# Kernel optimization log

Hardware: AMD Instinct MI355X
Metric: run time of the kernel (lower is better)

Reference implementation:

```python
import jax, jax.numpy as jnp
import numpy as np

EPS = 1e-12  # torch F.normalize eps


def setup_inputs() -> dict:
    key = jax.random.key(0)
    k1, k2, k3 = jax.random.split(key, 3)
    B, D, H, W, K = 64, 512, 32, 32, 64
    x = jax.random.normal(k1, (B, D, H, W), dtype=jnp.float32)
    w = jax.random.normal(k2, (K, D), dtype=jnp.float32) * 0.05  # 1x1 conv weight
    c = jax.random.normal(k3, (K, D), dtype=jnp.float32)          # cluster centers
    return {"x": x, "w": w, "c": c}


def reference(x, w, c):
    B, D, H, W = x.shape
    K = w.shape[0]
    N = H * W
    # 1x1 conv (no bias): (B,D,H,W) x (K,D) -> (B,K,H,W)
    features = jnp.einsum('bdhw,kd->bkhw', x, w)
    # NOTE: original applies softmax over dim=2 (the H axis only)
    a_bar = jax.nn.softmax(features, axis=2)
    xf = x.reshape(B, D, N)
    a = a_bar.reshape(B, K, N)
    # V[b,k,d] = sum_n a[b,k,n] * (x[b,d,n] - c[k,d])
    V = jnp.einsum('bkn,bdn->bkd', a, xf) - a.sum(axis=2)[:, :, None] * c[None]
    V = V.transpose(2, 1, 0)  # (D, K, B)
    # F.normalize(V, p=2, dim=1) applied twice (second is idempotent)
    norm = jnp.maximum(jnp.linalg.norm(V, axis=1, keepdims=True), EPS)
    y = V / norm
    norm2 = jnp.maximum(jnp.linalg.norm(y, axis=1, keepdims=True), EPS)
    return y / norm2
```

## Files before the change

kernel.cpp:

```cpp
#include <hip/hip_runtime.h>


typedef __attribute__((ext_vector_type(8))) short short8;
typedef __attribute__((ext_vector_type(4))) float f32x4;
typedef unsigned short u16;
typedef unsigned int u32;

union S8u { u32 q[4]; short8 s; };

__device__ __forceinline__ u32 pk2(float lo, float hi) {
  union { float f; u32 u; } a, b; a.f = lo; b.f = hi;
  u32 xl = (a.u + 0x7fffu + ((a.u >> 16) & 1u)) >> 16;
  u32 xh = (b.u + 0x7fffu + ((b.u >> 16) & 1u)) & 0xffff0000u;
  return xl | xh;
}

__device__ __forceinline__ u16 bf1(float f) {
  union { float f; u32 u; } a; a.f = f;
  return (u16)((a.u + 0x7fffu + ((a.u >> 16) & 1u)) >> 16);
}

__global__ __launch_bounds__(256, 2) void k1_features(
    const float* __restrict__ x, const float* __restrict__ wgt,
    float* __restrict__ feat)
{
  const int blk = blockIdx.x;
  const int b = blk & 63, ntile = blk >> 6;
  const int tid = threadIdx.x, lane = tid & 63, wv = tid >> 6;
  const int row = lane & 15, q = lane >> 4;
  const int nb = ntile * 128 + wv * 32;
  const float* xb = x + ((size_t)b << 19);

  f32x4 acc[4][2];
#pragma unroll
  for (int mt = 0; mt < 4; mt++)
#pragma unroll
    for (int nt = 0; nt < 2; nt++) acc[mt][nt] = (f32x4){0.f, 0.f, 0.f, 0.f};

#pragma unroll 2
  for (int d0 = 0; d0 < 512; d0 += 32) {
    short8 af[4];
#pragma unroll
    for (int mt = 0; mt < 4; mt++) {
      const float* pw = wgt + (mt * 16 + row) * 512 + d0 + q * 8;
      f32x4 w0 = *(const f32x4*)pw;
      f32x4 w1 = *(const f32x4*)(pw + 4);
      S8u t;
      t.q[0] = pk2(w0[0], w0[1]); t.q[1] = pk2(w0[2], w0[3]);
      t.q[2] = pk2(w1[0], w1[1]); t.q[3] = pk2(w1[2], w1[3]);
      af[mt] = t.s;
    }
    short8 bf[2];
#pragma unroll
    for (int nt = 0; nt < 2; nt++) {
      const float* px = xb + (size_t)(d0 + q * 8) * 1024 + nb + nt * 16 + row;
      float v0 = px[0],    v1 = px[1024], v2 = px[2048], v3 = px[3072];
      float v4 = px[4096], v5 = px[5120], v6 = px[6144], v7 = px[7168];
      S8u t;
      t.q[0] = pk2(v0, v1); t.q[1] = pk2(v2, v3);
      t.q[2] = pk2(v4, v5); t.q[3] = pk2(v6, v7);
      bf[nt] = t.s;
    }
#pragma unroll
    for (int nt = 0; nt < 2; nt++)
#pragma unroll
      for (int mt = 0; mt < 4; mt++)
        acc[mt][nt] = __builtin_amdgcn_mfma_f32_16x16x32_bf16(af[mt], bf[nt], acc[mt][nt], 0, 0, 0);
  }
  float* fb = feat + ((size_t)b << 16);
#pragma unroll
  for (int mt = 0; mt < 4; mt++)
#pragma unroll
    for (int nt = 0; nt < 2; nt++)
#pragma unroll
      for (int r = 0; r < 4; r++)
        fb[(mt * 16 + q * 4 + r) * 1024 + nb + nt * 16 + row] = acc[mt][nt][r];
}

__global__ __launch_bounds__(256) void k1b_softmax(
    const float* __restrict__ feat, u16* __restrict__ am)
{
  const int tid = threadIdx.x, lane = tid & 63, wv = tid >> 6;
  const int rid = blockIdx.x * 4 + wv;
  const float* f = feat + ((size_t)rid << 10);
  u16* ar = am + ((size_t)rid << 10);
  const int w = lane & 31, half = lane >> 5;
  const int base = w + half * 512;
  float v[16];
  float m = -1e30f;
#pragma unroll
  for (int i = 0; i < 16; i++) { v[i] = f[base + i * 32]; m = fmaxf(m, v[i]); }
  m = fmaxf(m, __shfl_xor(m, 32));
  float s = 0.f;
#pragma unroll
  for (int i = 0; i < 16; i++) { v[i] = __expf(v[i] - m); s += v[i]; }
  s += __shfl_xor(s, 32);
  const float inv = 1.0f / s;
#pragma unroll
  for (int i = 0; i < 16; i++) ar[base + i * 32] = bf1(v[i] * inv);
}

__global__ __launch_bounds__(256, 2) void k2_aggregate(
    const float* __restrict__ x, const u16* __restrict__ am,
    const float* __restrict__ cc, float* __restrict__ yw)
{
  const int blk = blockIdx.x;
  const int b = blk & 63, dt = blk >> 6;
  const int tid = threadIdx.x, lane = tid & 63, wv = tid >> 6;
  const int row = lane & 15, q = lane >> 4;
  const int drow = dt * 64 + wv * 16 + row;
  const float* xb = x + ((size_t)b << 19);
  const u16* ab = am + ((size_t)b << 16);

  f32x4 acc[4];
#pragma unroll
  for (int mt = 0; mt < 4; mt++) acc[mt] = (f32x4){0.f, 0.f, 0.f, 0.f};

#pragma unroll 2
  for (int n0 = 0; n0 < 1024; n0 += 32) {
    short8 bfr;
    {
      const float* px = xb + (size_t)drow * 1024 + n0 + q * 8;
      f32x4 g0 = *(const f32x4*)px;
      f32x4 g1 = *(const f32x4*)(px + 4);
      S8u t;
      t.q[0] = pk2(g0[0], g0[1]); t.q[1] = pk2(g0[2], g0[3]);
      t.q[2] = pk2(g1[0], g1[1]); t.q[3] = pk2(g1[2], g1[3]);
      bfr = t.s;
    }
#pragma unroll
    for (int mt = 0; mt < 4; mt++) {
      short8 af = *(const short8*)(ab + (mt * 16 + row) * 1024 + n0 + q * 8);
      acc[mt] = __builtin_amdgcn_mfma_f32_16x16x32_bf16(af, bfr, acc[mt], 0, 0, 0);
    }
  }
  const int dcol = dt * 64 + wv * 16 + row;
  float v[16]; float ss = 0.f;
#pragma unroll
  for (int mt = 0; mt < 4; mt++)
#pragma unroll
    for (int r = 0; r < 4; r++) {
      const int k = mt * 16 + q * 4 + r;
      const float t = acc[mt][r] - 32.0f * cc[k * 512 + dcol];
      v[mt * 4 + r] = t; ss += t * t;
    }
  ss += __shfl_xor(ss, 16);
  ss += __shfl_xor(ss, 32);
  const float rn = 1.0f / fmaxf(sqrtf(ss), 1e-12f);
  float* yb = yw + ((size_t)b << 15) + dcol;
#pragma unroll
  for (int mt = 0; mt < 4; mt++)
#pragma unroll
    for (int r = 0; r < 4; r++)
      yb[(size_t)(mt * 16 + q * 4 + r) << 9] = v[mt * 4 + r] * rn;
}

__global__ __launch_bounds__(256) void k3_transpose(
    const float* __restrict__ yw, float* __restrict__ out)
{
  const int blk = blockIdx.x;
  const int k = blk & 63;
  const int dt = blk >> 6;
  const int d0 = dt * 64;
  const int tid = threadIdx.x;
  __shared__ float T[64][68];
  {
    const int bl = tid >> 2, seg = tid & 3;
    const float* src = yw + (size_t)bl * 32768 + k * 512 + d0 + seg * 16;
#pragma unroll
    for (int i = 0; i < 4; i++) {
      f32x4 v = *(const f32x4*)(src + i * 4);
#pragma unroll
      for (int jj = 0; jj < 4; jj++) T[seg * 16 + i * 4 + jj][bl] = v[jj];
    }
  }
  __syncthreads();
  {
    const int dl = tid >> 2, bseg = tid & 3;
    float* dst = out + (size_t)(d0 + dl) * 4096 + k * 64 + bseg * 16;
    const float* srcT = &T[dl][bseg * 16];
#pragma unroll
    for (int i = 0; i < 4; i++)
      *(f32x4*)(dst + i * 4) = *(const f32x4*)(srcT + i * 4);
  }
}

extern "C" void kernel_launch(void* const* d_in, const int* in_sizes, int n_in,
                              void* d_out, int out_size, void* d_ws, size_t ws_size,
                              hipStream_t stream) {
  const float* x = (const float*)d_in[0];
  const float* w = (const float*)d_in[1];
  const float* c = (const float*)d_in[2];
  float* out = (float*)d_out;
  float* feat = (float*)d_ws;
  u16*   a_ws = (u16*)((char*)d_ws + (size_t)16 * 1024 * 1024);
  float* yw   = (float*)((char*)d_ws + (size_t)24 * 1024 * 1024);
  k1_features <<<dim3(512),  dim3(256), 0, stream>>>(x, w, feat);
  k1b_softmax <<<dim3(1024), dim3(256), 0, stream>>>(feat, a_ws);
  k2_aggregate<<<dim3(512),  dim3(256), 0, stream>>>(x, a_ws, c, yw);
  k3_transpose<<<dim3(512),  dim3(256), 0, stream>>>(yw, out);
}
```

Before: 274.4 us.

## Double-buffer GEMM operands through LDS with direct global-to-LDS loads

```diff
diff --git a/kernel.cpp b/kernel.cpp
--- a/kernel.cpp
+++ b/kernel.cpp
@@ -20,16 +20,39 @@
   return (u16)((a.u + 0x7fffu + ((a.u >> 16) & 1u)) >> 16);
 }
 
+typedef const __attribute__((address_space(1))) u32 GU32;
+typedef __attribute__((address_space(3))) u32 LU32;
+__device__ __forceinline__ void glds16(const void* g, void* l) {
+  __builtin_amdgcn_global_load_lds((GU32*)g, (LU32*)l, 16, 0, 0);
+}
+
+__global__ __launch_bounds__(256) void k0_packw(
+    const float* __restrict__ w, u16* __restrict__ wsw)
+{
+  const int tg = blockIdx.x * 256 + threadIdx.x;
+  const int dd4 = tg & 7, i = (tg >> 3) & 15, k = tg >> 7;
+  f32x4 v = *(const f32x4*)(w + k * 512 + i * 32 + dd4 * 4);
+  u32* dst = (u32*)(wsw + ((size_t)i * 64 + k) * 40 + dd4 * 4);
+  dst[0] = pk2(v[0], v[1]);
+  dst[1] = pk2(v[2], v[3]);
+}
+
 __global__ __launch_bounds__(256, 2) void k1_features(
-    const float* __restrict__ x, const float* __restrict__ wgt,
+    const float* __restrict__ x, const u16* __restrict__ wsw,
     float* __restrict__ feat)
 {
   const int blk = blockIdx.x;
-  const int b = blk & 63, ntile = blk >> 6;
+  const int b = blk & 63, nt8 = blk >> 6;
+  const int nb = nt8 * 128;
   const int tid = threadIdx.x, lane = tid & 63, wv = tid >> 6;
   const int row = lane & 15, q = lane >> 4;
-  const int nb = ntile * 128 + wv * 32;
-  const float* xb = x + ((size_t)b << 19);
+
+  __shared__ __align__(16) float xs[2][32][128];
+  __shared__ __align__(16) u16 wls[2][64][40];
+
+  const char* xbase = (const char*)(x + ((size_t)b << 19) + nb);
+  const char* wbase = (const char*)wsw;
+  const int dd0 = tid >> 5, cby = (tid & 31) * 16;
 
   f32x4 acc[4][2];
 #pragma unroll
@@ -37,53 +60,71 @@
 #pragma unroll
     for (int nt = 0; nt < 2; nt++) acc[mt][nt] = (f32x4){0.f, 0.f, 0.f, 0.f};
 
-#pragma unroll 2
-  for (int d0 = 0; d0 < 512; d0 += 32) {
+#define STAGE1(d0, buf)                                                        \
+  {                                                                            \
+    char* lx = (char*)&xs[buf][0][0];                                          \
+    _Pragma("unroll")                                                          \
+    for (int j = 0; j < 4; j++) {                                              \
+      const int dd = j * 8 + dd0;                                              \
+      glds16(xbase + (size_t)((d0) + dd) * 4096 + cby,                         \
+             lx + j * 4096 + tid * 16);                                        \
+    }                                                                          \
+    char* lw = (char*)&wls[buf][0][0];                                         \
+    const char* gw = wbase + (size_t)((d0) >> 5) * 5120;                       \
+    glds16(gw + tid * 16, lw + tid * 16);                                      \
+    if (tid < 64) glds16(gw + 4096 + tid * 16, lw + 4096 + tid * 16);          \
+  }
+
+  STAGE1(0, 0);
+  for (int i = 0; i < 16; i++) {
+    const int buf = i & 1;
+    __syncthreads();
+    if (i < 15) STAGE1((i + 1) * 32, buf ^ 1);
+
     short8 af[4];
 #pragma unroll
-    for (int mt = 0; mt < 4; mt++) {
-      const float* pw = wgt + (mt * 16 + row) * 512 + d0 + q * 8;
-      f32x4 w0 = *(const f32x4*)pw;
-      f32x4 w1 = *(const f32x4*)(pw + 4);
-      S8u t;
-      t.q[0] = pk2(w0[0], w0[1]); t.q[1] = pk2(w0[2], w0[3]);
-      t.q[2] = pk2(w1[0], w1[1]); t.q[3] = pk2(w1[2], w1[3]);
-      af[mt] = t.s;
-    }
-    short8 bf[2];
+    for (int mt = 0; mt < 4; mt++)
+      af[mt] = *(const short8*)&wls[buf][mt * 16 + row][q * 8];
+    short8 bfv[2];
 #pragma unroll
     for (int nt = 0; nt < 2; nt++) {
-      const float* px = xb + (size_t)(d0 + q * 8) * 1024 + nb + nt * 16 + row;
-      float v0 = px[0],    v1 = px[1024], v2 = px[2048], v3 = px[3072];
-      float v4 = px[4096], v5 = px[5120], v6 = px[6144], v7 = px[7168];
+      const int n = wv * 32 + nt * 16 + row;
+      const int d8 = q * 8;
+      float v0 = xs[buf][d8 + 0][n], v1 = xs[buf][d8 + 1][n];
+      float v2 = xs[buf][d8 + 2][n], v3 = xs[buf][d8 + 3][n];
+      float v4 = xs[buf][d8 + 4][n], v5 = xs[buf][d8 + 5][n];
+      float v6 = xs[buf][d8 + 6][n], v7 = xs[buf][d8 + 7][n];
       S8u t;
       t.q[0] = pk2(v0, v1); t.q[1] = pk2(v2, v3);
       t.q[2] = pk2(v4, v5); t.q[3] = pk2(v6, v7);
-      bf[nt] = t.s;
+      bfv[nt] = t.s;
     }
 #pragma unroll
     for (int nt = 0; nt < 2; nt++)
 #pragma unroll
       for (int mt = 0; mt < 4; mt++)
-        acc[mt][nt] = __builtin_amdgcn_mfma_f32_16x16x32_bf16(af[mt], bf[nt], acc[mt][nt], 0, 0, 0);
-  }
+        acc[mt][nt] = __builtin_amdgcn_mfma_f32_16x16x32_bf16(af[mt], bfv[nt], acc[mt][nt], 0, 0, 0);
+  }
+#undef STAGE1
+
   float* fb = feat + ((size_t)b << 16);
+  const int nbw = nb + wv * 32;
 #pragma unroll
   for (int mt = 0; mt < 4; mt++)
 #pragma unroll
     for (int nt = 0; nt < 2; nt++)
 #pragma unroll
       for (int r = 0; r < 4; r++)
-        fb[(mt * 16 + q * 4 + r) * 1024 + nb + nt * 16 + row] = acc[mt][nt][r];
+        fb[(mt * 16 + q * 4 + r) * 1024 + nbw + nt * 16 + row] = acc[mt][nt][r];
 }
 
 __global__ __launch_bounds__(256) void k1b_softmax(
-    const float* __restrict__ feat, u16* __restrict__ am)
+    const float* __restrict__ feat, u16* __restrict__ apad)
 {
   const int tid = threadIdx.x, lane = tid & 63, wv = tid >> 6;
   const int rid = blockIdx.x * 4 + wv;
+  const int b = rid >> 6, k = rid & 63;
   const float* f = feat + ((size_t)rid << 10);
-  u16* ar = am + ((size_t)rid << 10);
   const int w = lane & 31, half = lane >> 5;
   const int base = w + half * 512;
   float v[16];
@@ -97,43 +138,63 @@
   s += __shfl_xor(s, 32);
   const float inv = 1.0f / s;
 #pragma unroll
-  for (int i = 0; i < 16; i++) ar[base + i * 32] = bf1(v[i] * inv);
+  for (int i = 0; i < 16; i++) {
+    const int h = half * 16 + i;
+    apad[((size_t)(b * 32 + h) * 64 + k) * 40 + w] = bf1(v[i] * inv);
+  }
 }
 
 __global__ __launch_bounds__(256, 2) void k2_aggregate(
-    const float* __restrict__ x, const u16* __restrict__ am,
+    const float* __restrict__ x, const u16* __restrict__ apad,
     const float* __restrict__ cc, float* __restrict__ yw)
 {
   const int blk = blockIdx.x;
   const int b = blk & 63, dt = blk >> 6;
   const int tid = threadIdx.x, lane = tid & 63, wv = tid >> 6;
   const int row = lane & 15, q = lane >> 4;
-  const int drow = dt * 64 + wv * 16 + row;
-  const float* xb = x + ((size_t)b << 19);
-  const u16* ab = am + ((size_t)b << 16);
+
+  __shared__ __align__(16) u16 als[2][64][40];
+
+  const char* abase = (const char*)(apad + (size_t)b * 32 * 64 * 40);
+  const float* px0 = x + ((size_t)b << 19) + (size_t)(dt * 64 + wv * 16 + row) * 1024 + q * 8;
+
+#define STAGEA(i, buf)                                                         \
+  {                                                                            \
+    char* la = (char*)&als[buf][0][0];                                         \
+    const char* ga = abase + (size_t)(i) * 5120;                               \
+    glds16(ga + tid * 16, la + tid * 16);                                      \
+    if (tid < 64) glds16(ga + 4096 + tid * 16, la + 4096 + tid * 16);          \
+  }
 
   f32x4 acc[4];
 #pragma unroll
   for (int mt = 0; mt < 4; mt++) acc[mt] = (f32x4){0.f, 0.f, 0.f, 0.f};
 
-#pragma unroll 2
-  for (int n0 = 0; n0 < 1024; n0 += 32) {
-    short8 bfr;
-    {
-      const float* px = xb + (size_t)drow * 1024 + n0 + q * 8;
-      f32x4 g0 = *(const f32x4*)px;
-      f32x4 g1 = *(const f32x4*)(px + 4);
-      S8u t;
-      t.q[0] = pk2(g0[0], g0[1]); t.q[1] = pk2(g0[2], g0[3]);
-      t.q[2] = pk2(g1[0], g1[1]); t.q[3] = pk2(g1[2], g1[3]);
-      bfr = t.s;
-    }
+  STAGEA(0, 0);
+  f32x4 c0 = *(const f32x4*)px0;
+  f32x4 c1 = *(const f32x4*)(px0 + 4);
+  f32x4 p0, p1;
+  for (int i = 0; i < 32; i++) {
+    const int buf = i & 1;
+    __syncthreads();
+    if (i < 31) {
+      STAGEA(i + 1, buf ^ 1);
+      p0 = *(const f32x4*)(px0 + (i + 1) * 32);
+      p1 = *(const f32x4*)(px0 + (i + 1) * 32 + 4);
+    }
+    S8u t;
+    t.q[0] = pk2(c0[0], c0[1]); t.q[1] = pk2(c0[2], c0[3]);
+    t.q[2] = pk2(c1[0], c1[1]); t.q[3] = pk2(c1[2], c1[3]);
+    const short8 bfv = t.s;
 #pragma unroll
     for (int mt = 0; mt < 4; mt++) {
-      short8 af = *(const short8*)(ab + (mt * 16 + row) * 1024 + n0 + q * 8);
-      acc[mt] = __builtin_amdgcn_mfma_f32_16x16x32_bf16(af, bfr, acc[mt], 0, 0, 0);
-    }
-  }
+      short8 af = *(const short8*)&als[buf][mt * 16 + row][q * 8];
+      acc[mt] = __builtin_amdgcn_mfma_f32_16x16x32_bf16(af, bfv, acc[mt], 0, 0, 0);
+    }
+    c0 = p0; c1 = p1;
+  }
+#undef STAGEA
+
   const int dcol = dt * 64 + wv * 16 + row;
   float v[16]; float ss = 0.f;
 #pragma unroll
@@ -141,8 +202,8 @@
 #pragma unroll
     for (int r = 0; r < 4; r++) {
       const int k = mt * 16 + q * 4 + r;
-      const float t = acc[mt][r] - 32.0f * cc[k * 512 + dcol];
-      v[mt * 4 + r] = t; ss += t * t;
+      const float tv = acc[mt][r] - 32.0f * cc[k * 512 + dcol];
+      v[mt * 4 + r] = tv; ss += tv * tv;
     }
   ss += __shfl_xor(ss, 16);
   ss += __shfl_xor(ss, 32);
@@ -192,11 +253,14 @@
   const float* w = (const float*)d_in[1];
   const float* c = (const float*)d_in[2];
   float* out = (float*)d_out;
-  float* feat = (float*)d_ws;
-  u16*   a_ws = (u16*)((char*)d_ws + (size_t)16 * 1024 * 1024);
-  float* yw   = (float*)((char*)d_ws + (size_t)24 * 1024 * 1024);
-  k1_features <<<dim3(512),  dim3(256), 0, stream>>>(x, w, feat);
-  k1b_softmax <<<dim3(1024), dim3(256), 0, stream>>>(feat, a_ws);
-  k2_aggregate<<<dim3(512),  dim3(256), 0, stream>>>(x, a_ws, c, yw);
+  char* ws = (char*)d_ws;
+  float* feat = (float*)ws;
+  u16*   apad = (u16*)(ws + (size_t)16 * 1024 * 1024);
+  float* yw   = (float*)(ws + (size_t)26 * 1024 * 1024);
+  u16*   wsw  = (u16*)(ws + (size_t)34 * 1024 * 1024);
+  k0_packw    <<<dim3(32),   dim3(256), 0, stream>>>(w, wsw);
+  k1_features <<<dim3(512),  dim3(256), 0, stream>>>(x, wsw, feat);
+  k1b_softmax <<<dim3(1024), dim3(256), 0, stream>>>(feat, apad);
+  k2_aggregate<<<dim3(512),  dim3(256), 0, stream>>>(x, apad, c, yw);
   k3_transpose<<<dim3(512),  dim3(256), 0, stream>>>(yw, out);
 }
```

After: 231.9 us. 15.5% less time.
